# Kernel optimization log

Hardware: AMD Instinct MI355X
Metric: run time of the kernel (lower is better)

The kernel has to match this reference:

```python
import jax, jax.numpy as jnp
import numpy as np

B, C, D = 4096, 8192, 512
TEMP = 0.07
GAMMA_NEG, GAMMA_POS, CLIP, EPS = 4.0, 1.0, 0.05, 1e-8
NUM_ITERS = 5


def _l2norm(x):
    return x / jnp.linalg.norm(x, axis=-1, keepdims=True)


def setup_inputs() -> dict:
    key = jax.random.key(0)
    k1, k2, k3, k4 = jax.random.split(key, 4)
    features = _l2norm(jax.random.normal(k1, (B, D), jnp.float32))
    text_features = _l2norm(jax.random.normal(k2, (C, D), jnp.float32))
    targets = jax.random.uniform(k3, (B, C), dtype=jnp.float32)
    dataset_indices = jax.random.randint(k4, (B,), 0, 2, dtype=jnp.int32)
    return {"features": features, "text_features": text_features,
            "targets": targets, "dataset_indices": dataset_indices}


def iterate_P(P, sim_matrix, m, num_iterations=NUM_ITERS):
    # Faithful translation: note torch.diag on the [B,C] scaling_factors
    # extracts its main diagonal (length B since B<=C).
    for _ in range(num_iterations):
        column_sums_P = P.sum(axis=0)                         # [C]
        scaling_factors = jnp.minimum(sim_matrix / column_sums_P, 1.0)  # [B,C]
        d = jnp.diagonal(scaling_factors)                     # [B]
        P = P * d[:, None]
        P = P * (m / P.sum())
    return P


def _asym_loss(x, t):
    # AsymmetricLossOptimized (ASL) with gamma_neg=4, gamma_pos=1, clip=0.05
    xs_pos = jax.nn.sigmoid(x)
    xs_neg = jnp.minimum(1.0 - xs_pos + CLIP, 1.0)  # clip applied to negatives
    loss = t * jnp.log(jnp.maximum(xs_pos, EPS)) + (1.0 - t) * jnp.log(jnp.maximum(xs_neg, EPS))
    pt = xs_pos * t + xs_neg * (1.0 - t)
    gamma = GAMMA_POS * t + GAMMA_NEG * (1.0 - t)
    loss = loss * jnp.power(1.0 - pt, gamma)
    return -loss.sum()


def _forward(features, text_features, targets, dataset_indices):
    sim_matrix = (features @ text_features.T) / TEMP          # [B,C]
    P0 = jnp.exp(sim_matrix)
    cifar = (dataset_indices == 1)
    coco = (dataset_indices == 0)
    m = cifar.sum().astype(jnp.float32) + coco.sum().astype(jnp.float32) * 0.1
    P = iterate_P(P0, sim_matrix, m, NUM_ITERS)
    # cross_entropy with soft (probability) targets, mean over batch
    logp = jax.nn.log_softmax(P, axis=-1)
    multiclass_loss = -(targets * logp).sum(axis=-1).mean()
    multilabel_loss = _asym_loss(sim_matrix, targets)
    total_loss = multiclass_loss + multilabel_loss
    # row-masked sim matrices (jit-safe stand-in for data-dependent row gather)
    coco_sim = jnp.where(coco[:, None], sim_matrix, 0.0)
    cifar_sim = jnp.where(cifar[:, None], sim_matrix, 0.0)
    return total_loss, multiclass_loss, multilabel_loss, coco_sim, cifar_sim


def reference(features, text_features, targets, dataset_indices):
    return _forward(features, text_features, targets, dataset_indices)
```

## Files before the change

kernel.cpp:

```cpp
#include <hip/hip_runtime.h>
#include <stdint.h>

#define NB 4096
#define NC 8192
#define ND 512
#define INV_TEMP (1.0f/0.07f)

typedef float  f32x4 __attribute__((ext_vector_type(4)));
typedef unsigned int u32x4 __attribute__((ext_vector_type(4)));

__device__ __forceinline__ unsigned short f2bf(float f) {
    unsigned int u = __float_as_uint(f);
    u += 0x7fffu + ((u >> 16) & 1u);
    return (unsigned short)(u >> 16);
}
__device__ __forceinline__ float bflo(unsigned int u) {
    return __uint_as_float(u << 16);
}
__device__ __forceinline__ float bfhi(unsigned int u) {
    return __uint_as_float(u & 0xFFFF0000u);
}

__global__ __launch_bounds__(1024) void k_init(const int* __restrict__ idx,
                                               float* __restrict__ colsum,
                                               float* __restrict__ rv,
                                               float* __restrict__ scal) {
    __shared__ int red[1024];
    const int tid = threadIdx.x;
    int cnt = 0;
    for (int q = tid; q < NB; q += 1024) {
        colsum[q] = 0.f;
        rv[q] = 1.f;
        cnt += (idx[q] == 1) ? 1 : 0;
    }
    red[tid] = cnt; __syncthreads();
    for (int s = 512; s > 0; s >>= 1) {
        if (tid < s) red[tid] += red[tid + s];
        __syncthreads();
    }
    if (tid == 0) {
        const int c1 = red[0];
        scal[0] = (float)c1 + 0.1f * (float)(NB - c1);
        scal[1] = 0.f;
        scal[2] = 0.f;
    }
}

__global__ __launch_bounds__(256) void k_cvt(const float4* __restrict__ src,
                                             unsigned short* __restrict__ dst, int n4) {
    const int i = blockIdx.x * 256 + threadIdx.x;
    if (i >= n4) return;
    const float4 v = src[i];
    union { unsigned short h[4]; uint2 u; } p;
    p.h[0] = f2bf(v.x); p.h[1] = f2bf(v.y); p.h[2] = f2bf(v.z); p.h[3] = f2bf(v.w);
    ((uint2*)dst)[i] = p.u;
}

__global__ __launch_bounds__(256) void k_gemm(const unsigned short* __restrict__ Fb,
                                              const unsigned short* __restrict__ Tb,
                                              const int* __restrict__ idx,
                                              float* __restrict__ sim,
                                              float* __restrict__ coco,
                                              float* __restrict__ cifar,
                                              int fused) {
    __shared__ unsigned short lA[128 * 64];
    __shared__ unsigned short lB[128 * 64];
    const int tid  = threadIdx.x;
    const int lane = tid & 63;
    const int wid  = tid >> 6;
    const int wm = wid >> 1, wn = wid & 1;
    const int brow = blockIdx.y * 128;
    const int bcol = blockIdx.x * 128;

    f32x4 acc[4][4] = {};

    for (int kt = 0; kt < ND / 64; ++kt) {
        if (kt) __syncthreads();
#pragma unroll
        for (int c = 0; c < 4; ++c) {
            const int ch  = c * 4 + wid;
            const int o   = ch * 1024 + lane * 16;
            const int row = o >> 7;
            const int kbu = (o & 127) ^ ((row & 7) << 4);
            const unsigned short* gA = Fb + ((size_t)(brow + row) << 9) + (kt << 5)*2 + (kbu >> 1);
            __builtin_amdgcn_global_load_lds(
                (const __attribute__((address_space(1))) unsigned int*)gA,
                (__attribute__((address_space(3))) unsigned int*)((char*)lA + ch * 1024),
                16, 0, 0);
            const unsigned short* gB = Tb + ((size_t)(bcol + row) << 9) + (kt << 5)*2 + (kbu >> 1);
            __builtin_amdgcn_global_load_lds(
                (const __attribute__((address_space(1))) unsigned int*)gB,
                (__attribute__((address_space(3))) unsigned int*)((char*)lB + ch * 1024),
                16, 0, 0);
        }
        __syncthreads();
#pragma unroll
        for (int ks = 0; ks < 2; ++ks) {
            u32x4 af[4], bfr[4];
#pragma unroll
            for (int mi = 0; mi < 4; ++mi) {
                const int row  = wm * 64 + mi * 16 + (lane & 15);
                const int kb   = ks * 64 + ((lane >> 4) << 4);
                const int addr = row * 128 + (kb ^ ((row & 7) << 4));
                af[mi] = *(const u32x4*)((const char*)lA + addr);
            }
#pragma unroll
            for (int ni = 0; ni < 4; ++ni) {
                const int row  = wn * 64 + ni * 16 + (lane & 15);
                const int kb   = ks * 64 + ((lane >> 4) << 4);
                const int addr = row * 128 + (kb ^ ((row & 7) << 4));
                bfr[ni] = *(const u32x4*)((const char*)lB + addr);
            }
#pragma unroll
            for (int mi = 0; mi < 4; ++mi)
#pragma unroll
                for (int ni = 0; ni < 4; ++ni)
                    asm("v_mfma_f32_16x16x32_bf16 %0, %1, %2, %0"
                        : "+v"(acc[mi][ni]) : "v"(af[mi]), "v"(bfr[ni]));
        }
    }
    asm volatile("s_nop 7\n\ts_nop 7\n\ts_nop 7" ::);
    if (fused) {
#pragma unroll
        for (int mi = 0; mi < 4; ++mi) {
            const int rb = brow + wm * 64 + mi * 16 + ((lane >> 4) << 2);
            int fl[4];
#pragma unroll
            for (int rr = 0; rr < 4; ++rr) fl[rr] = (idx[rb + rr] == 1);
#pragma unroll
            for (int ni = 0; ni < 4; ++ni) {
                const int col = bcol + wn * 64 + ni * 16 + (lane & 15);
#pragma unroll
                for (int rr = 0; rr < 4; ++rr) {
                    const float s = acc[mi][ni][rr] * INV_TEMP;
                    const size_t o = (size_t)(rb + rr) * NC + col;
                    coco[o]  = fl[rr] ? 0.0f : s;
                    cifar[o] = fl[rr] ? s : 0.0f;
                }
            }
        }
    } else {
#pragma unroll
        for (int mi = 0; mi < 4; ++mi) {
            const int rb = brow + wm * 64 + mi * 16 + ((lane >> 4) << 2);
#pragma unroll
            for (int ni = 0; ni < 4; ++ni) {
                const int col = bcol + wn * 64 + ni * 16 + (lane & 15);
#pragma unroll
                for (int rr = 0; rr < 4; ++rr)
                    sim[(size_t)(rb + rr) * NC + col] = acc[mi][ni][rr] * INV_TEMP;
            }
        }
    }
}

__global__ __launch_bounds__(256) void k_stats(const float* __restrict__ pc,
                                               const float* __restrict__ pf,
                                               const int* __restrict__ idx,
                                               const float* __restrict__ tgt,
                                               unsigned short* __restrict__ Ebf,
                                               float* __restrict__ rowsum0,
                                               float* __restrict__ simdiag,
                                               float* __restrict__ Arow,
                                               float* __restrict__ Tsumv,
                                               float* __restrict__ rowmx,
                                               float* __restrict__ rowmn,
                                               float* __restrict__ scal) {
    const int i = blockIdx.x, tid = threadIdx.x;
    const float* srow = ((idx[i] == 1) ? pf : pc) + (size_t)i * NC;
    const float* trow = tgt + (size_t)i * NC;
    unsigned short* erow = Ebf ? (Ebf + (size_t)i * NC) : nullptr;
    float rs = 0.f, a = 0.f, ts = 0.f, ls = 0.f;
    float mx = -3.4e38f, mn = 3.4e38f;
    for (int c = tid * 4; c < NC; c += 1024) {
        const float s0 = srow[c], s1 = srow[c+1], s2 = srow[c+2], s3 = srow[c+3];
        const float4 t4 = *(const float4*)(trow + c);
        const float t0 = t4.x, t1 = t4.y, t2 = t4.z, t3 = t4.w;
        if ((unsigned)(i - c) < 4u)
            simdiag[i] = (i == c) ? s0 : ((i == c+1) ? s1 : ((i == c+2) ? s2 : s3));
        float e0, e1, e2, e3;
#define ASL(sv, tv, ev) { \
        ev = __expf(sv); \
        rs += ev; a += (tv) * ev; ts += (tv); \
        mx = fmaxf(mx, (sv)); mn = fminf(mn, (sv)); \
        const float inv = __builtin_amdgcn_rcpf(1.0f + ev); \
        const float xsp = ev * inv; \
        const float xsn = fminf(1.05f - xsp, 1.0f); \
        const float lp  = __logf(xsp); \
        const float ln  = __logf(xsn); \
        const float pt  = xsn + (tv) * (xsp - xsn); \
        const float g   = 4.0f - 3.0f * (tv); \
        const float pw  = __builtin_amdgcn_exp2f(g * __builtin_amdgcn_logf(1.0f - pt)); \
        ls += (ln + (tv) * (lp - ln)) * pw; }
        ASL(s0, t0, e0) ASL(s1, t1, e1) ASL(s2, t2, e2) ASL(s3, t3, e3)
#undef ASL
        if (erow) {
            uint2 w;
            w.x = (unsigned)f2bf(e0) | ((unsigned)f2bf(e1) << 16);
            w.y = (unsigned)f2bf(e2) | ((unsigned)f2bf(e3) << 16);
            *(uint2*)(erow + c) = w;
        }
    }
#pragma unroll
    for (int off = 1; off < 64; off <<= 1) {
        rs += __shfl_xor(rs, off);
        a  += __shfl_xor(a , off);
        ts += __shfl_xor(ts, off);
        ls += __shfl_xor(ls, off);
        mx = fmaxf(mx, __shfl_xor(mx, off));
        mn = fminf(mn, __shfl_xor(mn, off));
    }
    __shared__ float red[4][6];
    if ((tid & 63) == 0) {
        const int w = tid >> 6;
        red[w][0] = rs; red[w][1] = a; red[w][2] = ts;
        red[w][3] = ls; red[w][4] = mx; red[w][5] = mn;
    }
    __syncthreads();
    if (tid == 0) {
        rowsum0[i] = red[0][0] + red[1][0] + red[2][0] + red[3][0];
        Arow[i]    = red[0][1] + red[1][1] + red[2][1] + red[3][1];
        Tsumv[i]   = red[0][2] + red[1][2] + red[2][2] + red[3][2];
        atomicAdd(&scal[1], red[0][3] + red[1][3] + red[2][3] + red[3][3]);
        rowmx[i] = fmaxf(fmaxf(red[0][4], red[1][4]), fmaxf(red[2][4], red[3][4]));
        rowmn[i] = fminf(fminf(red[0][5], red[1][5]), fminf(red[2][5], red[3][5]));
    }
}

__global__ __launch_bounds__(256) void k_colsum_e(const unsigned short* __restrict__ Ebf,
                                                  const float* __restrict__ rv,
                                                  float* __restrict__ colsum) {
    const int j  = (blockIdx.x * 256 + threadIdx.x) * 4;
    const int i0 = blockIdx.y * 64;
    float a0 = 0.f, a1 = 0.f, a2 = 0.f, a3 = 0.f;
    for (int i = i0; i < i0 + 64; ++i) {
        const uint2 u = *(const uint2*)(Ebf + (size_t)i * NC + j);
        const float r = rv[i];
        a0 += bflo(u.x) * r;
        a1 += bfhi(u.x) * r;
        a2 += bflo(u.y) * r;
        a3 += bfhi(u.y) * r;
    }
    atomicAdd(&colsum[j    ], a0);
    atomicAdd(&colsum[j + 1], a1);
    atomicAdd(&colsum[j + 2], a2);
    atomicAdd(&colsum[j + 3], a3);
}

__global__ __launch_bounds__(256) void k_colsum(const float* __restrict__ pc,
                                                const float* __restrict__ pf,
                                                const int* __restrict__ idx,
                                                const float* __restrict__ rv,
                                                float* __restrict__ colsum) {
    const int j  = (blockIdx.x * 256 + threadIdx.x) * 4;
    const int i0 = blockIdx.y * 32;
    float a0 = 0.f, a1 = 0.f, a2 = 0.f, a3 = 0.f;
    for (int i = i0; i < i0 + 32; ++i) {
        const float* row = ((idx[i] == 1) ? pf : pc) + (size_t)i * NC;
        const float r = rv[i];
        a0 += __expf(row[j    ]) * r;
        a1 += __expf(row[j + 1]) * r;
        a2 += __expf(row[j + 2]) * r;
        a3 += __expf(row[j + 3]) * r;
    }
    atomicAdd(&colsum[j    ], a0);
    atomicAdd(&colsum[j + 1], a1);
    atomicAdd(&colsum[j + 2], a2);
    atomicAdd(&colsum[j + 3], a3);
}

__global__ __launch_bounds__(1024) void k_update(const float* __restrict__ simdiag,
                                                 float* __restrict__ colsum,
                                                 const float* __restrict__ rowsum0,
                                                 float* __restrict__ rv,
                                                 const float* __restrict__ scal) {
    __shared__ float red[1024];
    const int tid = threadIdx.x;
    float part = 0.f;
    float rl[4];
#pragma unroll
    for (int q = 0; q < 4; ++q) {
        const int i = tid + q * 1024;
        const float d  = fminf(simdiag[i] / colsum[i], 1.0f);
        const float rn = rv[i] * d;
        rl[q] = rn;
        part += rn * rowsum0[i];
        colsum[i] = 0.f;
    }
    red[tid] = part; __syncthreads();
    for (int s = 512; s > 0; s >>= 1) {
        if (tid < s) red[tid] += red[tid + s];
        __syncthreads();
    }
    const float sc = scal[0] / red[0];
#pragma unroll
    for (int q = 0; q < 4; ++q) rv[tid + q * 1024] = rl[q] * sc;
}

__global__ __launch_bounds__(256) void k_rowfinal_e(const unsigned short* __restrict__ Ebf,
                                                    const float* __restrict__ rv,
                                                    const float* __restrict__ Arow,
                                                    const float* __restrict__ Tsumv,
                                                    const float* __restrict__ rowmx,
                                                    const float* __restrict__ rowmn,
                                                    float* __restrict__ scal) {
    const int i = blockIdx.x, tid = threadIdx.x;
    const float ri = rv[i];
    const unsigned short* erow = Ebf + (size_t)i * NC;
    const float M = ri * __expf((ri >= 0.f) ? rowmx[i] : rowmn[i]);
    float se = 0.f;
    for (int c = tid * 8; c < NC; c += 2048) {
        const uint4 u = *(const uint4*)(erow + c);
        se += __expf(ri * bflo(u.x) - M);
        se += __expf(ri * bfhi(u.x) - M);
        se += __expf(ri * bflo(u.y) - M);
        se += __expf(ri * bfhi(u.y) - M);
        se += __expf(ri * bflo(u.z) - M);
        se += __expf(ri * bfhi(u.z) - M);
        se += __expf(ri * bflo(u.w) - M);
        se += __expf(ri * bfhi(u.w) - M);
    }
#pragma unroll
    for (int off = 1; off < 64; off <<= 1) se += __shfl_xor(se, off);
    __shared__ float red[4];
    if ((tid & 63) == 0) red[tid >> 6] = se;
    __syncthreads();
    if (tid == 0) {
        const float L = M + __logf(red[0] + red[1] + red[2] + red[3]);
        atomicAdd(&scal[2], Tsumv[i] * L - ri * Arow[i]);
    }
}

__global__ __launch_bounds__(256) void k_rowfinal(const float* __restrict__ pc,
                                                  const float* __restrict__ pf,
                                                  const int* __restrict__ idx,
                                                  const float* __restrict__ rv,
                                                  const float* __restrict__ Arow,
                                                  const float* __restrict__ Tsumv,
                                                  const float* __restrict__ rowmx,
                                                  const float* __restrict__ rowmn,
                                                  float* __restrict__ scal) {
    const int i = blockIdx.x, tid = threadIdx.x;
    const float ri = rv[i];
    const float* srow = ((idx[i] == 1) ? pf : pc) + (size_t)i * NC;
    const float M = ri * __expf((ri >= 0.f) ? rowmx[i] : rowmn[i]);
    float se = 0.f;
    for (int c = tid * 4; c < NC; c += 1024) {
        se += __expf(ri * __expf(srow[c    ]) - M);
        se += __expf(ri * __expf(srow[c + 1]) - M);
        se += __expf(ri * __expf(srow[c + 2]) - M);
        se += __expf(ri * __expf(srow[c + 3]) - M);
    }
#pragma unroll
    for (int off = 1; off < 64; off <<= 1) se += __shfl_xor(se, off);
    __shared__ float red[4];
    if ((tid & 63) == 0) red[tid >> 6] = se;
    __syncthreads();
    if (tid == 0) {
        const float L = M + __logf(red[0] + red[1] + red[2] + red[3]);
        atomicAdd(&scal[2], Tsumv[i] * L - ri * Arow[i]);
    }
}

__global__ void k_scalars(const float* __restrict__ scal, float* __restrict__ out) {
    if (threadIdx.x == 0) {
        const float mc = scal[2] / (float)NB;
        const float ml = -scal[1];
        out[0] = mc + ml;
        out[1] = mc;
        out[2] = ml;
    }
}

__global__ __launch_bounds__(256) void k_mask(const float* sim, const int* idx,
                                              float* coco, float* cifar) {
    const int i = blockIdx.y;
    const int c = blockIdx.x * 256 + threadIdx.x;
    const size_t o = (size_t)i * NC + c;
    const float s = sim[o];
    const bool isCifar = (idx[i] == 1);
    coco[o]  = isCifar ? 0.0f : s;
    cifar[o] = isCifar ? s : 0.0f;
}

extern "C" void kernel_launch(void* const* d_in, const int* in_sizes, int n_in,
                              void* d_out, int out_size, void* d_ws, size_t ws_size,
                              hipStream_t stream) {
    const float* F   = (const float*)d_in[0];
    const float* T   = (const float*)d_in[1];
    const float* tgt = (const float*)d_in[2];
    const int*   idx = (const int*)d_in[3];

    float* out   = (float*)d_out;
    float* coco  = out + 3;
    float* cifar = coco + (size_t)NB * NC;

    const size_t FbBytes    = (size_t)NB * ND * 2;
    const size_t TbBytes    = (size_t)NC * ND * 2;
    const size_t EBytes     = (size_t)NB * NC * 2;
    const size_t smallBytes = 10 * (size_t)NB * 4 + 1024;

    const bool fused = (d_ws != nullptr) &&
                       (ws_size >= FbBytes + TbBytes + smallBytes + 512);
    const bool hasE  = (d_ws != nullptr) &&
                       (ws_size >= FbBytes + TbBytes + EBytes + smallBytes + 512);
    unsigned short *Fb, *Tb, *Ebf = nullptr;
    float *sm, *sim;
    if (fused) {
        Fb  = (unsigned short*)d_ws;
        Tb  = (unsigned short*)((char*)d_ws + FbBytes);
        char* p = (char*)d_ws + FbBytes + TbBytes;
        if (hasE) { Ebf = (unsigned short*)p; p += EBytes; }
        sm  = (float*)p;
        sim = nullptr;
    } else {
        sim = cifar;
        char* base = (char*)(((uintptr_t)(void*)coco + 255) & ~(uintptr_t)255);
        Fb  = (unsigned short*)base;
        Tb  = (unsigned short*)(base + FbBytes);
        sm  = (float*)(base + FbBytes + TbBytes);
    }
    float* colsum  = sm;
    float* rv      = sm + NB;
    float* rowsum0 = sm + 2 * NB;
    float* simdiag = sm + 3 * NB;
    float* Arow    = sm + 4 * NB;
    float* Tsumv   = sm + 5 * NB;
    float* rowmx   = sm + 6 * NB;
    float* rowmn   = sm + 7 * NB;
    float* scal    = sm + 8 * NB;

    const float* pc = fused ? coco  : sim;
    const float* pf = fused ? cifar : sim;

    k_init<<<1, 1024, 0, stream>>>(idx, colsum, rv, scal);
    k_cvt<<<(NB * ND / 4) / 256, 256, 0, stream>>>((const float4*)F, Fb, NB * ND / 4);
    k_cvt<<<(NC * ND / 4) / 256, 256, 0, stream>>>((const float4*)T, Tb, NC * ND / 4);
    k_gemm<<<dim3(NC / 128, NB / 128), 256, 0, stream>>>(Fb, Tb, idx, sim, coco, cifar,
                                                         fused ? 1 : 0);
    k_stats<<<NB, 256, 0, stream>>>(pc, pf, idx, tgt, Ebf, rowsum0, simdiag, Arow, Tsumv,
                                    rowmx, rowmn, scal);
    for (int it = 0; it < 5; ++it) {
        if (hasE)
            k_colsum_e<<<dim3(NB / 1024, 64), 256, 0, stream>>>(Ebf, rv, colsum);
        else
            k_colsum<<<dim3(NB / 1024, 128), 256, 0, stream>>>(pc, pf, idx, rv, colsum);
        k_update<<<1, 1024, 0, stream>>>(simdiag, colsum, rowsum0, rv, scal);
    }
    if (hasE)
        k_rowfinal_e<<<NB, 256, 0, stream>>>(Ebf, rv, Arow, Tsumv, rowmx, rowmn, scal);
    else
        k_rowfinal<<<NB, 256, 0, stream>>>(pc, pf, idx, rv, Arow, Tsumv, rowmx, rowmn, scal);
    k_scalars<<<1, 64, 0, stream>>>(scal, out);
    if (!fused) k_mask<<<dim3(NC / 256, NB), 256, 0, stream>>>(sim, idx, coco, cifar);
}
```

Measured before the change: 334.6 us.

## Fuse row statistics, masking and first column sum into the GEMM epilogue

On the path that keeps a bf16 exp matrix, the GEMM epilogue now writes the masked coco/cifar outputs directly. It also computes per-row sums, max/min (via ordered-int atomics), the asymmetric loss partials and the first column sum, and stores the bf16 exp tile. This removes the separate stats kernel and extra passes over the full similarity matrix. Later iterations merge the column-sum and update kernels using a last-block-done counter, and the two conversion kernels are merged into one. The cost is heavy epilogue work and many atomics inside the GEMM, which may raise register pressure.

```diff
diff --git a/kernel.cpp b/kernel.cpp
--- a/kernel.cpp
+++ b/kernel.cpp
@@ -19,6 +19,46 @@
 }
 __device__ __forceinline__ float bfhi(unsigned int u) {
     return __uint_as_float(u & 0xFFFF0000u);
+}
+__device__ __forceinline__ unsigned int fenc(float f) {
+    const unsigned int u = __float_as_uint(f);
+    return (u & 0x80000000u) ? ~u : (u | 0x80000000u);
+}
+__device__ __forceinline__ float fdec(unsigned int k) {
+    return __uint_as_float((k & 0x80000000u) ? (k ^ 0x80000000u) : ~k);
+}
+
+__global__ __launch_bounds__(1024) void k_init2(const int* __restrict__ idx,
+                                                float* __restrict__ colsum,
+                                                float* __restrict__ rv,
+                                                float* __restrict__ rowsum0,
+                                                float* __restrict__ Arow,
+                                                float* __restrict__ Tsumv,
+                                                unsigned int* __restrict__ rowmxK,
+                                                unsigned int* __restrict__ rowmnK,
+                                                float* __restrict__ scal) {
+    __shared__ int red[1024];
+    const int tid = threadIdx.x;
+    int cnt = 0;
+    for (int q = tid; q < NB; q += 1024) {
+        colsum[q] = 0.f; rv[q] = 1.f;
+        rowsum0[q] = 0.f; Arow[q] = 0.f; Tsumv[q] = 0.f;
+        rowmxK[q] = 0u; rowmnK[q] = 0xFFFFFFFFu;
+        cnt += (idx[q] == 1) ? 1 : 0;
+    }
+    red[tid] = cnt; __syncthreads();
+    for (int s = 512; s > 0; s >>= 1) {
+        if (tid < s) red[tid] += red[tid + s];
+        __syncthreads();
+    }
+    if (tid == 0) {
+        const int c1 = red[0];
+        scal[0] = (float)c1 + 0.1f * (float)(NB - c1);
+        scal[1] = 0.f;
+        scal[2] = 0.f;
+        unsigned int* u = (unsigned int*)scal;
+        u[4] = 0u; u[5] = 0u; u[6] = 0u; u[7] = 0u; u[8] = 0u;
+    }
 }
 
 __global__ __launch_bounds__(1024) void k_init(const int* __restrict__ idx,
@@ -46,6 +86,19 @@
     }
 }
 
+__global__ __launch_bounds__(256) void k_cvt2(const float4* __restrict__ F4,
+                                              const float4* __restrict__ T4,
+                                              unsigned short* __restrict__ Fb,
+                                              unsigned short* __restrict__ Tb) {
+    const int i  = blockIdx.x * 256 + threadIdx.x;
+    const int nF = NB * ND / 4;
+    const float4 v = (i < nF) ? F4[i] : T4[i - nF];
+    union { unsigned short h[4]; uint2 u; } p;
+    p.h[0] = f2bf(v.x); p.h[1] = f2bf(v.y); p.h[2] = f2bf(v.z); p.h[3] = f2bf(v.w);
+    if (i < nF) ((uint2*)Fb)[i] = p.u;
+    else        ((uint2*)Tb)[i - nF] = p.u;
+}
+
 __global__ __launch_bounds__(256) void k_cvt(const float4* __restrict__ src,
                                              unsigned short* __restrict__ dst, int n4) {
     const int i = blockIdx.x * 256 + threadIdx.x;
@@ -54,6 +107,165 @@
     union { unsigned short h[4]; uint2 u; } p;
     p.h[0] = f2bf(v.x); p.h[1] = f2bf(v.y); p.h[2] = f2bf(v.z); p.h[3] = f2bf(v.w);
     ((uint2*)dst)[i] = p.u;
+}
+
+__global__ __launch_bounds__(256) void k_gemm_fused(const unsigned short* __restrict__ Fb,
+                                                    const unsigned short* __restrict__ Tb,
+                                                    const int* __restrict__ idx,
+                                                    const float* __restrict__ tgt,
+                                                    float* __restrict__ coco,
+                                                    float* __restrict__ cifar,
+                                                    unsigned short* __restrict__ Ebf,
+                                                    float* __restrict__ colsum,
+                                                    float* __restrict__ rowsum0,
+                                                    float* __restrict__ simdiag,
+                                                    float* __restrict__ Arow,
+                                                    float* __restrict__ Tsumv,
+                                                    unsigned int* __restrict__ rowmxK,
+                                                    unsigned int* __restrict__ rowmnK,
+                                                    float* __restrict__ scal) {
+    __shared__ unsigned short lds[128 * 128];
+    __shared__ float lsred[4];
+    unsigned short* lA = lds;
+    unsigned short* lB = lds + 128 * 64;
+    const int tid  = threadIdx.x;
+    const int lane = tid & 63;
+    const int wid  = tid >> 6;
+    const int wm = wid >> 1, wn = wid & 1;
+    const int brow = blockIdx.y * 128;
+    const int bcol = blockIdx.x * 128;
+
+    f32x4 acc[4][4] = {};
+
+    for (int kt = 0; kt < ND / 64; ++kt) {
+        if (kt) __syncthreads();
+#pragma unroll
+        for (int c = 0; c < 4; ++c) {
+            const int ch  = c * 4 + wid;
+            const int o   = ch * 1024 + lane * 16;
+            const int row = o >> 7;
+            const int kbu = (o & 127) ^ ((row & 7) << 4);
+            const unsigned short* gA = Fb + ((size_t)(brow + row) << 9) + (kt << 5)*2 + (kbu >> 1);
+            __builtin_amdgcn_global_load_lds(
+                (const __attribute__((address_space(1))) unsigned int*)gA,
+                (__attribute__((address_space(3))) unsigned int*)((char*)lA + ch * 1024),
+                16, 0, 0);
+            const unsigned short* gB = Tb + ((size_t)(bcol + row) << 9) + (kt << 5)*2 + (kbu >> 1);
+            __builtin_amdgcn_global_load_lds(
+                (const __attribute__((address_space(1))) unsigned int*)gB,
+                (__attribute__((address_space(3))) unsigned int*)((char*)lB + ch * 1024),
+                16, 0, 0);
+        }
+        __syncthreads();
+#pragma unroll
+        for (int ks = 0; ks < 2; ++ks) {
+            u32x4 af[4], bfr[4];
+#pragma unroll
+            for (int mi = 0; mi < 4; ++mi) {
+                const int row  = wm * 64 + mi * 16 + (lane & 15);
+                const int kb   = ks * 64 + ((lane >> 4) << 4);
+                const int addr = row * 128 + (kb ^ ((row & 7) << 4));
+                af[mi] = *(const u32x4*)((const char*)lA + addr);
+            }
+#pragma unroll
+            for (int ni = 0; ni < 4; ++ni) {
+                const int row  = wn * 64 + ni * 16 + (lane & 15);
+                const int kb   = ks * 64 + ((lane >> 4) << 4);
+                const int addr = row * 128 + (kb ^ ((row & 7) << 4));
+                bfr[ni] = *(const u32x4*)((const char*)lB + addr);
+            }
+#pragma unroll
+            for (int mi = 0; mi < 4; ++mi)
+#pragma unroll
+                for (int ni = 0; ni < 4; ++ni)
+                    asm("v_mfma_f32_16x16x32_bf16 %0, %1, %2, %0"
+                        : "+v"(acc[mi][ni]) : "v"(af[mi]), "v"(bfr[ni]));
+        }
+    }
+    asm volatile("s_nop 7\n\ts_nop 7\n\ts_nop 7" ::);
+    __syncthreads();
+
+    const int r0    = (lane >> 4) << 2;
+    const int cl0   = wn * 64 + (lane & 15);
+    float ls = 0.f;
+    float colp[4] = {0.f, 0.f, 0.f, 0.f};
+#pragma unroll
+    for (int mi = 0; mi < 4; ++mi) {
+        const int rl0 = wm * 64 + mi * 16 + r0;
+#pragma unroll
+        for (int rr = 0; rr < 4; ++rr) {
+            const int rl  = rl0 + rr;
+            const int row = brow + rl;
+            const int isC = (idx[row] == 1);
+            float rs = 0.f, a = 0.f, ts = 0.f;
+            float mx = -3.4e38f, mn = 3.4e38f;
+#pragma unroll
+            for (int ni = 0; ni < 4; ++ni) {
+                const int cl  = cl0 + ni * 16;
+                const int col = bcol + cl;
+                const float s = acc[mi][ni][rr] * INV_TEMP;
+                const size_t o = (size_t)row * NC + col;
+                coco[o]  = isC ? 0.0f : s;
+                cifar[o] = isC ? s    : 0.0f;
+                const float t = tgt[o];
+                const float e = __expf(s);
+                const unsigned short eb = f2bf(e);
+                lds[rl * 128 + cl] = eb;
+                if (row == col) simdiag[row] = s;
+                rs += e; a += t * e; ts += t;
+                mx = fmaxf(mx, s); mn = fminf(mn, s);
+                colp[ni] += __uint_as_float((unsigned int)eb << 16);
+                const float inv = __builtin_amdgcn_rcpf(1.0f + e);
+                const float xsp = e * inv;
+                const float xsn = fminf(1.05f - xsp, 1.0f);
+                const float lp  = __logf(xsp);
+                const float ln  = __logf(xsn);
+                const float pt  = xsn + t * (xsp - xsn);
+                const float g   = 4.0f - 3.0f * t;
+                const float pw  = __builtin_amdgcn_exp2f(g * __builtin_amdgcn_logf(1.0f - pt));
+                ls += (ln + t * (lp - ln)) * pw;
+            }
+#pragma unroll
+            for (int off = 1; off < 16; off <<= 1) {
+                rs += __shfl_xor(rs, off);
+                a  += __shfl_xor(a,  off);
+                ts += __shfl_xor(ts, off);
+                mx = fmaxf(mx, __shfl_xor(mx, off));
+                mn = fminf(mn, __shfl_xor(mn, off));
+            }
+            if ((lane & 15) == 0) {
+                atomicAdd(&rowsum0[row], rs);
+                atomicAdd(&Arow[row],    a);
+                atomicAdd(&Tsumv[row],   ts);
+                atomicMax(&rowmxK[row], fenc(mx));
+                atomicMin(&rowmnK[row], fenc(mn));
+            }
+        }
+    }
+    if (bcol < NB) {
+#pragma unroll
+        for (int ni = 0; ni < 4; ++ni) {
+            colp[ni] += __shfl_xor(colp[ni], 16);
+            colp[ni] += __shfl_xor(colp[ni], 32);
+        }
+        if (lane < 16) {
+#pragma unroll
+            for (int ni = 0; ni < 4; ++ni)
+                atomicAdd(&colsum[bcol + wn * 64 + ni * 16 + lane], colp[ni]);
+        }
+    }
+#pragma unroll
+    for (int off = 1; off < 64; off <<= 1) ls += __shfl_xor(ls, off);
+    if (lane == 0) lsred[wid] = ls;
+    __syncthreads();
+    if (tid == 0) atomicAdd(&scal[1], lsred[0] + lsred[1] + lsred[2] + lsred[3]);
+#pragma unroll
+    for (int p = 0; p < 8; ++p) {
+        const int cidx = tid + p * 256;
+        const int r = cidx >> 4, ch = cidx & 15;
+        *(uint4*)((char*)(Ebf + (size_t)(brow + r) * NC + bcol) + ch * 16) =
+            *(const uint4*)((const char*)lds + r * 256 + ch * 16);
+    }
 }
 
 __global__ __launch_bounds__(256) void k_gemm(const unsigned short* __restrict__ Fb,
@@ -227,26 +439,6 @@
     }
 }
 
-__global__ __launch_bounds__(256) void k_colsum_e(const unsigned short* __restrict__ Ebf,
-                                                  const float* __restrict__ rv,
-                                                  float* __restrict__ colsum) {
-    const int j  = (blockIdx.x * 256 + threadIdx.x) * 4;
-    const int i0 = blockIdx.y * 64;
-    float a0 = 0.f, a1 = 0.f, a2 = 0.f, a3 = 0.f;
-    for (int i = i0; i < i0 + 64; ++i) {
-        const uint2 u = *(const uint2*)(Ebf + (size_t)i * NC + j);
-        const float r = rv[i];
-        a0 += bflo(u.x) * r;
-        a1 += bfhi(u.x) * r;
-        a2 += bflo(u.y) * r;
-        a3 += bfhi(u.y) * r;
-    }
-    atomicAdd(&colsum[j    ], a0);
-    atomicAdd(&colsum[j + 1], a1);
-    atomicAdd(&colsum[j + 2], a2);
-    atomicAdd(&colsum[j + 3], a3);
-}
-
 __global__ __launch_bounds__(256) void k_colsum(const float* __restrict__ pc,
                                                 const float* __restrict__ pf,
                                                 const int* __restrict__ idx,
@@ -297,17 +489,70 @@
     for (int q = 0; q < 4; ++q) rv[tid + q * 1024] = rl[q] * sc;
 }
 
-__global__ __launch_bounds__(256) void k_rowfinal_e(const unsigned short* __restrict__ Ebf,
-                                                    const float* __restrict__ rv,
-                                                    const float* __restrict__ Arow,
-                                                    const float* __restrict__ Tsumv,
-                                                    const float* __restrict__ rowmx,
-                                                    const float* __restrict__ rowmn,
-                                                    float* __restrict__ scal) {
+__global__ __launch_bounds__(256) void k_iter(const unsigned short* __restrict__ Ebf,
+                                              float* __restrict__ rv,
+                                              float* __restrict__ colsum,
+                                              const float* __restrict__ simdiag,
+                                              const float* __restrict__ rowsum0,
+                                              const float* __restrict__ scal,
+                                              unsigned int* __restrict__ cnt) {
+    const int tid = threadIdx.x;
+    const int j   = (blockIdx.x * 256 + tid) * 4;
+    const int i0  = blockIdx.y * 64;
+    float a0 = 0.f, a1 = 0.f, a2 = 0.f, a3 = 0.f;
+    for (int i = i0; i < i0 + 64; ++i) {
+        const uint2 u = *(const uint2*)(Ebf + (size_t)i * NC + j);
+        const float r = rv[i];
+        a0 += bflo(u.x) * r;
+        a1 += bfhi(u.x) * r;
+        a2 += bflo(u.y) * r;
+        a3 += bfhi(u.y) * r;
+    }
+    atomicAdd(&colsum[j    ], a0);
+    atomicAdd(&colsum[j + 1], a1);
+    atomicAdd(&colsum[j + 2], a2);
+    atomicAdd(&colsum[j + 3], a3);
+    __threadfence();
+    __shared__ int isLast;
+    __syncthreads();
+    if (tid == 0) isLast = (atomicAdd(cnt, 1u) == 255u);
+    __syncthreads();
+    if (!isLast) return;
+    __threadfence();
+    float part = 0.f;
+    float rl[16];
+#pragma unroll
+    for (int q = 0; q < 16; ++q) {
+        const int i = q * 256 + tid;
+        const float cs = atomicAdd(&colsum[i], 0.0f);
+        const float d  = fminf(simdiag[i] / cs, 1.0f);
+        const float rn = rv[i] * d;
+        rl[q] = rn;
+        part += rn * rowsum0[i];
+        colsum[i] = 0.f;
+    }
+#pragma unroll
+    for (int off = 1; off < 64; off <<= 1) part += __shfl_xor(part, off);
+    __shared__ float red[4];
+    if ((tid & 63) == 0) red[tid >> 6] = part;
+    __syncthreads();
+    const float S  = red[0] + red[1] + red[2] + red[3];
+    const float sc = scal[0] / S;
+#pragma unroll
+    for (int q = 0; q < 16; ++q) rv[q * 256 + tid] = rl[q] * sc;
+}
+
+__global__ __launch_bounds__(256) void k_rowfinal_e2(const unsigned short* __restrict__ Ebf,
+                                                     const float* __restrict__ rv,
+                                                     const float* __restrict__ Arow,
+                                                     const float* __restrict__ Tsumv,
+                                                     const unsigned int* __restrict__ rowmxK,
+                                                     const unsigned int* __restrict__ rowmnK,
+                                                     float* __restrict__ scal) {
     const int i = blockIdx.x, tid = threadIdx.x;
     const float ri = rv[i];
     const unsigned short* erow = Ebf + (size_t)i * NC;
-    const float M = ri * __expf((ri >= 0.f) ? rowmx[i] : rowmn[i]);
+    const float M = ri * __expf((ri >= 0.f) ? fdec(rowmxK[i]) : fdec(rowmnK[i]));
     float se = 0.f;
     for (int c = tid * 8; c < NC; c += 2048) {
         const uint4 u = *(const uint4*)(erow + c);
@@ -430,6 +675,26 @@
     float* rowmn   = sm + 7 * NB;
     float* scal    = sm + 8 * NB;
 
+    if (hasE) {
+        k_init2<<<1, 1024, 0, stream>>>(idx, colsum, rv, rowsum0, Arow, Tsumv,
+                                        (unsigned int*)rowmx, (unsigned int*)rowmn, scal);
+        k_cvt2<<<((NB + NC) * ND / 4) / 256, 256, 0, stream>>>((const float4*)F,
+                                                               (const float4*)T, Fb, Tb);
+        k_gemm_fused<<<dim3(NC / 128, NB / 128), 256, 0, stream>>>(
+            Fb, Tb, idx, tgt, coco, cifar, Ebf, colsum, rowsum0, simdiag, Arow, Tsumv,
+            (unsigned int*)rowmx, (unsigned int*)rowmn, scal);
+        k_update<<<1, 1024, 0, stream>>>(simdiag, colsum, rowsum0, rv, scal);
+        for (int it = 1; it < 5; ++it)
+            k_iter<<<dim3(NB / 1024, 64), 256, 0, stream>>>(Ebf, rv, colsum, simdiag,
+                                                            rowsum0, scal,
+                                                            (unsigned int*)scal + 4 + it);
+        k_rowfinal_e2<<<NB, 256, 0, stream>>>(Ebf, rv, Arow, Tsumv,
+                                              (const unsigned int*)rowmx,
+                                              (const unsigned int*)rowmn, scal);
+        k_scalars<<<1, 64, 0, stream>>>(scal, out);
+        return;
+    }
+
     const float* pc = fused ? coco  : sim;
     const float* pf = fused ? cifar : sim;
 
@@ -438,19 +703,13 @@
     k_cvt<<<(NC * ND / 4) / 256, 256, 0, stream>>>((const float4*)T, Tb, NC * ND / 4);
     k_gemm<<<dim3(NC / 128, NB / 128), 256, 0, stream>>>(Fb, Tb, idx, sim, coco, cifar,
                                                          fused ? 1 : 0);
-    k_stats<<<NB, 256, 0, stream>>>(pc, pf, idx, tgt, Ebf, rowsum0, simdiag, Arow, Tsumv,
+    k_stats<<<NB, 256, 0, stream>>>(pc, pf, idx, tgt, nullptr, rowsum0, simdiag, Arow, Tsumv,
                                     rowmx, rowmn, scal);
     for (int it = 0; it < 5; ++it) {
-        if (hasE)
-            k_colsum_e<<<dim3(NB / 1024, 64), 256, 0, stream>>>(Ebf, rv, colsum);
-        else
-            k_colsum<<<dim3(NB / 1024, 128), 256, 0, stream>>>(pc, pf, idx, rv, colsum);
+        k_colsum<<<dim3(NB / 1024, 128), 256, 0, stream>>>(pc, pf, idx, rv, colsum);
         k_update<<<1, 1024, 0, stream>>>(simdiag, colsum, rowsum0, rv, scal);
     }
-    if (hasE)
-        k_rowfinal_e<<<NB, 256, 0, stream>>>(Ebf, rv, Arow, Tsumv, rowmx, rowmn, scal);
-    else
-        k_rowfinal<<<NB, 256, 0, stream>>>(pc, pf, idx, rv, Arow, Tsumv, rowmx, rowmn, scal);
+    k_rowfinal<<<NB, 256, 0, stream>>>(pc, pf, idx, rv, Arow, Tsumv, rowmx, rowmn, scal);
     k_scalars<<<1, 64, 0, stream>>>(scal, out);
     if (!fused) k_mask<<<dim3(NC / 256, NB), 256, 0, stream>>>(sim, idx, coco, cifar);
 }
```

Measured after the change: 452.1 us. 1.35x slower.
